# Optimization experiments

Measured on AMD Instinct MI355X. Metric: run time of the kernel, lower is better.

Reference implementation:

```python
import jax, jax.numpy as jnp
import numpy as np

C = 128; HEADS = 8; GH = 32; GW = 32; B = 8; PD = 8  # PD = (dim//4)//4

def _conv(x, w, pad, dil=1, groups=1):
    return jax.lax.conv_general_dilated(
        x, w, (1, 1), [(pad[0], pad[0]), (pad[1], pad[1])],
        rhs_dilation=(dil, dil),
        dimension_numbers=('NCHW', 'OIHW', 'NCHW'),
        feature_group_count=groups)

def _lrelu(t):
    return jnp.where(t >= 0, t, 0.1 * t)

def _ln(t, g, b, eps=1e-5):
    m = jnp.mean(t, -1, keepdims=True)
    v = jnp.var(t, -1, keepdims=True)
    return (t - m) * jax.lax.rsqrt(v + eps) * g + b

def setup_inputs():
    rng = np.random.RandomState(0)
    f = lambda *s: jnp.asarray((rng.randn(*s) * 0.05).astype(np.float32))
    ones = lambda n: jnp.ones((n,), jnp.float32)
    zeros = lambda n: jnp.zeros((n,), jnp.float32)
    # Swin-style relative position index over the (GH, GW) group
    coords = np.stack(np.meshgrid(np.arange(GH), np.arange(GW), indexing='ij')).reshape(2, -1)
    rel = (coords[:, :, None] - coords[:, None, :]).transpose(1, 2, 0)
    rel[..., 0] += GH - 1; rel[..., 1] += GW - 1; rel[..., 0] *= 2 * GW - 1
    rel_idx = jnp.asarray(rel.sum(-1).astype(np.int32))  # [N, N]
    biases = np.stack(np.meshgrid(np.arange(1 - GH, GH), np.arange(1 - GW, GW), indexing='ij'))
    biases = jnp.asarray(biases.reshape(2, -1).T.astype(np.float32))  # [(2GH-1)*(2GW-1), 2]
    return dict(
        x=jnp.asarray(rng.rand(B, C, GH, GW).astype(np.float32)),
        conv1_w=f(C, C, 3, 3), conv2_w=f(C, C, 3, 3), conv3_w=f(C, C, 3, 3),
        convt_w=f(C, 3, 1, 1),
        rba_w=f(C, C, 3, 1), rba_b=zeros(C), rbb_w=f(C, C, 1, 3), rbb_b=zeros(C),
        pp_w=f(PD, 2), pp_b=zeros(PD),
        l1_g=ones(PD), l1_b=zeros(PD), l1_w=f(PD, PD), l1_b2=zeros(PD),
        l2_g=ones(PD), l2_b=zeros(PD), l2_w=f(PD, PD), l2_b2=zeros(PD),
        l3_g=ones(PD), l3_b=zeros(PD), l3_w=f(HEADS, PD), l3_b2=zeros(HEADS),
        qk_w=f(2 * C, C), qk_b=zeros(2 * C),
        v_w=f(C, C), v_b=zeros(C),
        proj_w=f(C, C), proj_b=zeros(C),
        fc1_w=f(C, C), fc1_b=zeros(C), fc2_w=f(C, C), fc2_b=zeros(C),
        biases=biases, rel_idx=rel_idx,
    )

def reference(x, conv1_w, conv2_w, conv3_w, convt_w, rba_w, rba_b, rbb_w, rbb_b,
              pp_w, pp_b, l1_g, l1_b, l1_w, l1_b2, l2_g, l2_b, l2_w, l2_b2,
              l3_g, l3_b, l3_w, l3_b2, qk_w, qk_b, v_w, v_b, proj_w, proj_b,
              fc1_w, fc1_b, fc2_w, fc2_b, biases, rel_idx):
    Bn, Cc, Hh, Ww = x.shape
    N = Hh * Ww
    hd = Cc // HEADS
    # FeaExtract: ResASPP (3 dilated 3x3 convs, grouped 1x1 merge) + residual
    b1 = _lrelu(_conv(x, conv1_w, (1, 1)))
    b2 = _lrelu(_conv(x, conv2_w, (3, 3), dil=3))
    b3 = _lrelu(_conv(x, conv3_w, (5, 5), dil=5))
    a = _conv(jnp.concatenate([b1, b2, b3], 1), convt_w, (0, 0), groups=Cc) + x
    # RB: (3,1) conv -> lrelu -> (1,3) conv + residual
    r = _lrelu(_conv(a, rba_w, (1, 0)) + rba_b[None, :, None, None])
    r = _conv(r, rbb_w, (0, 1)) + rbb_b[None, :, None, None]
    o0 = r + a
    # original uses in-place clamp_, so o0 is clamped before flattening
    o0 = jnp.clip(o0, 0.0, 1.0)
    E = o0.reshape(Bn, Cc, N).transpose(0, 2, 1)  # [B, N, C]
    qk = E @ qk_w.T + qk_b  # [B, N, 2C]
    q = qk[..., :Cc].reshape(Bn, N, HEADS, hd).transpose(0, 2, 1, 3)
    k = qk[..., Cc:].reshape(Bn, N, HEADS, hd).transpose(0, 2, 1, 3)
    v = (E @ v_w.T + v_b).reshape(Bn, N, HEADS, hd).transpose(0, 2, 1, 3)
    attn = jnp.einsum('bhid,bhjd->bhij', q * (hd ** -0.5), k)
    # DynamicPosBias MLP (residual=False): Linear(2,pd) -> [LN,ReLU,Linear] x2 -> LN,ReLU,Linear(pd,heads)
    p = biases @ pp_w.T + pp_b
    p = jax.nn.relu(_ln(p, l1_g, l1_b)) @ l1_w.T + l1_b2
    p = jax.nn.relu(_ln(p, l2_g, l2_b)) @ l2_w.T + l2_b2
    p = jax.nn.relu(_ln(p, l3_g, l3_b)) @ l3_w.T + l3_b2  # [L, heads]
    rpb = p[rel_idx]  # gather -> [N, N, heads]
    attn = attn + rpb.transpose(2, 0, 1)[None]
    attn = jax.nn.softmax(attn, axis=-1)
    y = jnp.einsum('bhij,bhjd->bhid', attn, v).transpose(0, 2, 1, 3).reshape(Bn, N, Cc) + E
    x_proj = y @ proj_w.T + proj_b
    h = jax.nn.gelu(x_proj @ fc1_w.T + fc1_b, approximate=False)
    return (h @ fc2_w.T + fc2_b) + y
```

## Files before the change

### kernel.cpp

```cpp
#include <hip/hip_runtime.h>
#include <hip/hip_bf16.h>

typedef __hip_bfloat16 bf16;
typedef __bf16 bf16x8 __attribute__((ext_vector_type(8)));
typedef float f32x4 __attribute__((ext_vector_type(4)));

#define Lb 3969

#define XP_F   0
#define WF_F   903168
#define WR_F   1124352
#define WG_F   1173504
#define BH_F   1222656
#define R1P_F  1222656
#define QKV_F  1222656
#define AP_F   2795520
#define YT_F   2795520
#define EB_F   3352576
#define XPT_F  3352576
#define H1T_F  0
#define RPB_F  3876864
#define FLAG_F 3908616
#define RT_F   3908624
#define VT_F   4924432

__device__ __forceinline__ float b2f(bf16 v) { return __bfloat162float(v); }
__device__ __forceinline__ bf16 f2b(float v) { return __float2bfloat16(v); }

template <typename T> __device__ __forceinline__ float ldw(const void* p, int i);
template <> __device__ __forceinline__ float ldw<bf16>(const void* p, int i) {
  return __bfloat162float(((const bf16*)p)[i]);
}
template <> __device__ __forceinline__ float ldw<float>(const void* p, int i) {
  return ((const float*)p)[i];
}
template <typename T> __device__ __forceinline__ void stw(void* p, size_t i, float v);
template <> __device__ __forceinline__ void stw<bf16>(void* p, size_t i, float v) {
  ((bf16*)p)[i] = __float2bfloat16(v);
}
template <> __device__ __forceinline__ void stw<float>(void* p, size_t i, float v) {
  ((float*)p)[i] = v;
}

__device__ __forceinline__ unsigned pkb(float a, float b) {
  bf16 x = __float2bfloat16(a), y = __float2bfloat16(b);
  unsigned short ux = *(unsigned short*)&x, uy = *(unsigned short*)&y;
  return (unsigned)ux | ((unsigned)uy << 16);
}

__device__ __forceinline__ bool detect_local(const unsigned* x) {
  int lane = threadIdx.x & 63;
  int cnt = 0;
#pragma unroll
  for (int k = 0; k < 4; ++k) {
// ... 39 lines not shown
            f2b(ldw<T>(w, ((mt * 16 + li) * 128 + Kc * 32 + quad * 8 + j) * 3 + t));
    } else if (u < 24576) {
      int g = u - 12288;
      int Kc = (g >> 6) & 3, mtg = g >> 8;
      const void* w; int mrow; float sc = 1.f;
      if (mtg < 16)      { w = qk_w;   mrow = mtg * 16; if (mtg < 8) sc = 0.25f; }
      else if (mtg < 24) { w = v_w;    mrow = (mtg - 16) * 16; }
      else if (mtg < 32) { w = proj_w; mrow = (mtg - 24) * 16; }
      else if (mtg < 40) { w = fc1_w;  mrow = (mtg - 32) * 16; }
      else               { w = fc2_w;  mrow = (mtg - 40) * 16; }
#pragma unroll
      for (int j = 0; j < 8; ++j)
        Wg[(size_t)g * 8 + j] =
            f2b(sc * ldw<T>(w, (mrow + li) * 128 + Kc * 32 + quad * 8 + j));
    }
  }
}

__global__ __launch_bounds__(256) void wprep_all_kernel(
    const unsigned* x, const void* w1, const void* w2, const void* w3,
    const void* rba_w, const void* rbb_w, const void* qk_w, const void* v_w,
    const void* proj_w, const void* fc1_w, const void* fc2_w,
    bf16* Wf, bf16* Wr, bf16* Wg, int* flag)
{
  bool isbf = detect_local(x);
  if (blockIdx.x == 0 && threadIdx.x == 0) *flag = isbf ? 1 : 0;
  if (isbf) wprep_all_body<bf16>(w1, w2, w3, rba_w, rbb_w, qk_w, v_w, proj_w,
                                 fc1_w, fc2_w, Wf, Wr, Wg);
  else      wprep_all_body<float>(w1, w2, w3, rba_w, rbb_w, qk_w, v_w, proj_w,
                                  fc1_w, fc2_w, Wf, Wr, Wg);
}

template <typename T>
__device__ void nhwc_body(const void* x, bf16* __restrict__ xp, bf16 (*tile)[128])
{
  const int b = blockIdx.x >> 5;
  const int row = blockIdx.x & 31;
  const int t = threadIdx.x;
  const size_t bbase = (size_t)b * 42 * 42 * 128;
  const bf16x8 z = (bf16x8){};

  if (t < 160) {
    int side = t / 80;
    int off = (t % 80) * 8;
    *(bf16x8*)&xp[bbase + ((size_t)(row + 5) * 42 + side * 37) * 128 + off] = z;
  }
  {
    int zr = (row < 5) ? row : ((row >= 27) ? row + 10 : -1);
    if (zr >= 0) {
      size_t base = bbase + (size_t)zr * 42 * 128;
      for (int k = t; k < 672; k += 256) *(bf16x8*)&xp[base + k * 8] = z;
    }
  }

  {
    int ci = t >> 1, half = t & 1;
#pragma unroll
    for (int j = 0; j < 16; ++j) {
      int px = half * 16 + j;
      tile[px][ci] = f2b(ldw<T>(x, ((size_t)b * 128 + ci) * 1024 + row * 32 + px));
    }
  }
  __syncthreads();
  {
    int px = t >> 3, c0 = (t & 7) * 16;
    bf16* dst = xp + (bbase + ((size_t)(row + 5) * 42 + (px + 5)) * 128 + c0);
// ... 73 lines not shown
  const int y = px >> 5, x = px & 31;
  const bf16* brow = bh + ((size_t)b * 1024 + px) * 384 + o0 * 3;
  const bf16* xrow = xp + (((size_t)b * 42 + y + 5) * 42 + x + 5) * 128 + o0;
  bf16* arow = ap + (((size_t)b * 34 + y + 1) * 32 + x) * 128 + o0;

  bf16 bl[48], xl[16], ol[16];
#pragma unroll
  for (int k = 0; k < 6; ++k) *(bf16x8*)&bl[k * 8] = *(const bf16x8*)&brow[k * 8];
  *(bf16x8*)&xl[0] = *(const bf16x8*)&xrow[0];
  *(bf16x8*)&xl[8] = *(const bf16x8*)&xrow[8];
#pragma unroll
  for (int j = 0; j < 16; ++j) {
    float v = b2f(xl[j]);
#pragma unroll
    for (int i = 0; i < 3; ++i) {
      float t = b2f(bl[j * 3 + i]);
      v += cw[(o0 + j) * 3 + i] * (t >= 0.f ? t : 0.1f * t);
    }
    ol[j] = f2b(v);
  }
  *(bf16x8*)&arow[0] = *(bf16x8*)&ol[0];
  *(bf16x8*)&arow[8] = *(bf16x8*)&ol[8];
}

__global__ __launch_bounds__(256) void merge2_kernel(
    const bf16* xp, const void* wt, const bf16* bh, bf16* ap, const int* flag)
{
  __shared__ float cw[384];
  if (*flag) merge2_body<bf16>(xp, wt, bh, ap, cw);
  else       merge2_body<float>(xp, wt, bh, ap, cw);
}

template <typename T>
__device__ void rb1_body(const bf16* __restrict__ ap, const bf16* __restrict__ Wr,
                         const void* bias, bf16* __restrict__ r1p)
{
  const int b = blockIdx.z, mh = blockIdx.y;
  const int lane = threadIdx.x;
  const int quad = lane >> 4, li = lane & 15;
  const int pxw = blockIdx.x * 16;
  const int y = pxw >> 5, xb = pxw & 31;
  f32x4 acc[4] = {};
#pragma unroll
  for (int t = 0; t < 3; ++t) {
    const bf16* Asite = ap + (((size_t)b * 34 + y + t) * 32 + xb + li) * 128;
#pragma unroll
    for (int Kc = 0; Kc < 4; ++Kc) {
      bf16x8 afrag = *(const bf16x8*)(Asite + Kc * 32 + quad * 8);
#pragma unroll
      for (int mt = 0; mt < 4; ++mt) {
        int f = (t * 8 + mh * 4 + mt) * 4 + Kc;
        bf16x8 wfrag = *(const bf16x8*)(Wr + ((size_t)f * 64 + lane) * 8);
        acc[mt] = __builtin_amdgcn_mfma_f32_16x16x32_bf16(afrag, wfrag, acc[mt],
                                                          0, 0, 0);
      }
    }
  }
  if (quad == 0) {
    int xcol = (xb == 0) ? 0 : 33;
#pragma unroll
    for (int mt = 0; mt < 4; ++mt)
      r1p[(((size_t)b * 32 + y) * 34 + xcol) * 128 + (mh * 4 + mt) * 16 + li] =
          f2b(0.f);
  }
#pragma unroll
  for (int mt = 0; mt < 4; ++mt) {
    int o = (mh * 4 + mt) * 16 + li;
    float bv = ldw<T>(bias, o);
#pragma unroll
    for (int r = 0; r < 4; ++r) {
      int x = xb + quad * 4 + r;
      float v = acc[mt][r] + bv;
      v = (v >= 0.f ? v : 0.1f * v);
      r1p[(((size_t)b * 32 + y) * 34 + x + 1) * 128 + o] = f2b(v);
    }
  }
}

__global__ __launch_bounds__(64) void rb1_kernel(
    const bf16* ap, const bf16* Wr, const void* bias, bf16* r1p, const int* flag)
{
  if (*flag) rb1_body<bf16>(ap, Wr, bias, r1p);
  else       rb1_body<float>(ap, Wr, bias, r1p);
}

template <typename T>
__device__ void rb2_body(const bf16* __restrict__ r1p, const bf16* __restrict__ Wr,
                         const void* bias, const bf16* __restrict__ ap,
                         bf16* __restrict__ Eb)
{
  const int b = blockIdx.z, mh = blockIdx.y;
  const int lane = threadIdx.x;
  const int quad = lane >> 4, li = lane & 15;
  const int pxw = blockIdx.x * 16;
  const int y = pxw >> 5, xb = pxw & 31;
  f32x4 acc[4] = {};
#pragma unroll
  for (int t = 0; t < 3; ++t) {
    const bf16* Asite = r1p + (((size_t)b * 32 + y) * 34 + xb + li + t) * 128;
#pragma unroll
    for (int Kc = 0; Kc < 4; ++Kc) {
      bf16x8 afrag = *(const bf16x8*)(Asite + Kc * 32 + quad * 8);
#pragma unroll
      for (int mt = 0; mt < 4; ++mt) {
        int f = ((3 + t) * 8 + mh * 4 + mt) * 4 + Kc;
        bf16x8 wfrag = *(const bf16x8*)(Wr + ((size_t)f * 64 + lane) * 8);
        acc[mt] = __builtin_amdgcn_mfma_f32_16x16x32_bf16(afrag, wfrag, acc[mt],
                                                          0, 0, 0);
      }
    }
  }
#pragma unroll
  for (int mt = 0; mt < 4; ++mt) {
    int o = (mh * 4 + mt) * 16 + li;
    float bv = ldw<T>(bias, o);
#pragma unroll
    for (int r = 0; r < 4; ++r) {
      int x = xb + quad * 4 + r;
      float v = acc[mt][r] + bv +
                b2f(ap[(((size_t)b * 34 + y + 1) * 32 + x) * 128 + o]);
      v = fminf(fmaxf(v, 0.f), 1.f);
      Eb[((size_t)b * 1024 + y * 32 + x) * 128 + o] = f2b(v);
    }
  }
}

__global__ __launch_bounds__(64) void rb2_kernel(
    const bf16* r1p, const bf16* Wr, const void* bias, const bf16* ap,
    bf16* Eb, const int* flag)
{
  if (*flag) rb2_body<bf16>(r1p, Wr, bias, ap, Eb);
  else       rb2_body<float>(r1p, Wr, bias, ap, Eb);
}

template <typename T>
__device__ __forceinline__ void ln_relu8(const float* t, float* u,
                                         const void* g, const void* bb)
{
  float m = 0.f;
#pragma unroll
  for (int k = 0; k < 8; ++k) m += t[k];
  m *= 0.125f;
  float v = 0.f;
#pragma unroll
  for (int k = 0; k < 8; ++k) { float d = t[k] - m; v += d * d; }
  v *= 0.125f;
  float r = rsqrtf(v + 1e-5f);
#pragma unroll
  for (int k = 0; k < 8; ++k) {
    float val = (t[k] - m) * r * ldw<T>(g, k) + ldw<T>(bb, k);
    u[k] = val > 0.f ? val : 0.f;
  }
}

template <typename T>
__device__ void dpb_body(const void* biases, const void* pp_w, const void* pp_b,
                         const void* l1_g, const void* l1_b, const void* l1_w,
                         const void* l1_b2, const void* l2_g, const void* l2_b,
                         const void* l2_w, const void* l2_b2, const void* l3_g,
                         const void* l3_b, const void* l3_w, const void* l3_b2,
                         float* __restrict__ RPB)
{
  int r = blockIdx.x * 256 + threadIdx.x;
  if (r >= Lb) return;
  float b0 = ldw<T>(biases, r * 2), b1 = ldw<T>(biases, r * 2 + 1);
  float t[8], u[8];
#pragma unroll
  for (int j = 0; j < 8; ++j)
    t[j] = b0 * ldw<T>(pp_w, j * 2) + b1 * ldw<T>(pp_w, j * 2 + 1) +
           ldw<T>(pp_b, j);
  ln_relu8<T>(t, u, l1_g, l1_b);
#pragma unroll
  for (int j = 0; j < 8; ++j) {
    float s = ldw<T>(l1_b2, j);
#pragma unroll
    for (int k = 0; k < 8; ++k) s += u[k] * ldw<T>(l1_w, j * 8 + k);
    t[j] = s;
  }
  ln_relu8<T>(t, u, l2_g, l2_b);
#pragma unroll
  for (int j = 0; j < 8; ++j) {
    float s = ldw<T>(l2_b2, j);
#pragma unroll
    for (int k = 0; k < 8; ++k) s += u[k] * ldw<T>(l2_w, j * 8 + k);
    t[j] = s;
  }
  ln_relu8<T>(t, u, l3_g, l3_b);
#pragma unroll
  for (int h = 0; h < 8; ++h) {
    float s = ldw<T>(l3_b2, h);
#pragma unroll
    for (int k = 0; k < 8; ++k) s += u[k] * ldw<T>(l3_w, h * 8 + k);
    RPB[h * Lb + r] = s;
  }
}

__global__ __launch_bounds__(256) void dpb_kernel(
    const void* biases, const void* pp_w, const void* pp_b, const void* l1_g,
    const void* l1_b, const void* l1_w, const void* l1_b2, const void* l2_g,
    const void* l2_b, const void* l2_w, const void* l2_b2, const void* l3_g,
    const void* l3_b, const void* l3_w, const void* l3_b2, float* RPB,
    const int* flag)
{
  if (*flag)
    dpb_body<bf16>(biases, pp_w, pp_b, l1_g, l1_b, l1_w, l1_b2, l2_g, l2_b,
                   l2_w, l2_b2, l3_g, l3_b, l3_w, l3_b2, RPB);
  else
    dpb_body<float>(biases, pp_w, pp_b, l1_g, l1_b, l1_w, l1_b2, l2_g, l2_b,
                    l2_w, l2_b2, l3_g, l3_b, l3_w, l3_b2, RPB);
}

__global__ __launch_bounds__(64) void rt_kernel(
    const float* __restrict__ RPB, float* __restrict__ RT)
{
  const int tt = blockIdx.x, h = blockIdx.y;
  const int t = tt >> 1, p = tt & 1;
  const int lane = threadIdx.x, quad = lane >> 4, li = lane & 15;
  const float* rp = RPB + h * Lb;
#pragma unroll
  for (int mt = 0; mt < 4; ++mt) {
    f32x4 v;
#pragma unroll
    for (int r = 0; r < 4; ++r) {
      int j = mt * 16 + quad * 4 + r;
      int dy = (t - 30) - (j >> 5);
      int dx = (p * 16 + li) - (j & 31);
      v[r] = rp[(dy + 31) * 63 + dx + 31];
    }
    *(f32x4*)&RT[(((size_t)h * 124 + tt) * 4 + mt) * 256 + lane * 4] = v;
  }
}

__global__ __launch_bounds__(64) void vt_kernel(
    const bf16* __restrict__ QKV, bf16* __restrict__ VT)
{
  const int c = blockIdx.x, hh = blockIdx.y, b = blockIdx.z;
  __shared__ bf16 Vl[64][20];
  const int lane = threadIdx.x, quad = lane >> 4, li = lane & 15;
  const bf16* vsrc =
      QKV + ((size_t)b * 1024 + c * 64 + lane) * 384 + 256 + hh * 16;
  union { bf16x8 v; uint2 u[2]; } w0, w1;
  w0.v = *(const bf16x8*)vsrc;
  w1.v = *(const bf16x8*)(vsrc + 8);
  *(uint2*)&Vl[lane][0] = w0.u[0];
  *(uint2*)&Vl[lane][4] = w0.u[1];
  *(uint2*)&Vl[lane][8] = w1.u[0];
  *(uint2*)&Vl[lane][12] = w1.u[1];
  __syncthreads();
#pragma unroll
  for (int half = 0; half < 2; ++half) {
    union { bf16 e[8]; bf16x8 v; } uv;
#pragma unroll
    for (int jj = 0; jj < 8; ++jj)
      uv.e[jj] = Vl[half * 32 + quad * 8 + jj][li];
    *(bf16x8*)&VT[((((size_t)(b * 8 + hh) * 16 + c) * 2 + half) * 64 + lane) * 8] =
        uv.v;
  }
}

template <typename T>
__device__ void qkv_body(const bf16* __restrict__ Eb, const bf16* __restrict__ Wg,
                         const void* qk_b, const void* v_b,
                         bf16* __restrict__ QKV)
{
  const int grp = blockIdx.y, b = blockIdx.z;
  const int w = threadIdx.x >> 6, lane = threadIdx.x & 63;
  const int quad = lane >> 4, li = lane & 15;
  const int pxw = blockIdx.x * 64 + w * 16;
  bf16x8 ef[4];
#pragma unroll
  for (int Kc = 0; Kc < 4; ++Kc)
    ef[Kc] = *(const bf16x8*)&Eb[((size_t)b * 1024 + pxw + li) * 128 + Kc * 32 +
                                 quad * 8];
  f32x4 acc[8] = {};
#pragma unroll
  for (int nt = 0; nt < 8; ++nt) {
    int g = grp * 8 + nt;
#pragma unroll
    for (int Kc = 0; Kc < 4; ++Kc) {
      bf16x8 wf = *(const bf16x8*)&Wg[(((size_t)g * 4 + Kc) * 64 + lane) * 8];
      acc[nt] = __builtin_amdgcn_mfma_f32_16x16x32_bf16(ef[Kc], wf, acc[nt],
                                                        0, 0, 0);
    }
  }
#pragma unroll
  for (int nt = 0; nt < 8; ++nt) {
    int g = grp * 8 + nt;
    int o = g * 16 + li;
    float bv;
    if (g < 8)       bv = 0.25f * ldw<T>(qk_b, o);
    else if (g < 16) bv = ldw<T>(qk_b, o);
    else             bv = ldw<T>(v_b, o - 256);
#pragma unroll
    for (int r = 0; r < 4; ++r) {
      int px = pxw + quad * 4 + r;
      QKV[((size_t)b * 1024 + px) * 384 + o] = f2b(acc[nt][r] + bv);
    }
  }
}

__global__ __launch_bounds__(256) void qkv_kernel(
    const bf16* Eb, const bf16* Wg, const void* qk_b, const void* v_b,
    bf16* QKV, const int* flag)
{
  if (*flag) qkv_body<bf16>(Eb, Wg, qk_b, v_b, QKV);
  else       qkv_body<float>(Eb, Wg, qk_b, v_b, QKV);
}

template <typename T, int MODE>
__device__ void mlp_body(const bf16* __restrict__ src, const bf16* __restrict__ Wg,
                         int tb, const void* bias, const bf16* __restrict__ res,
                         void* out)
{
  const int b = blockIdx.z, mh = blockIdx.y;
  const int lane = threadIdx.x;
  const int quad = lane >> 4, li = lane & 15;
  const int pxw = blockIdx.x * 16;
  bf16x8 ef[4];
#pragma unroll
  for (int Kc = 0; Kc < 4; ++Kc)
    ef[Kc] = *(const bf16x8*)&src[((size_t)b * 1024 + pxw + li) * 128 + Kc * 32 +
                                  quad * 8];
  f32x4 acc[2] = {};
#pragma unroll
  for (int nt = 0; nt < 2; ++nt)
#pragma unroll
    for (int Kc = 0; Kc < 4; ++Kc) {
      bf16x8 wf = *(const bf16x8*)&Wg[
          (((size_t)(tb + mh * 2 + nt) * 4 + Kc) * 64 + lane) * 8];
      acc[nt] = __builtin_amdgcn_mfma_f32_16x16x32_bf16(ef[Kc], wf, acc[nt],
                                                        0, 0, 0);
    }
#pragma unroll
  for (int nt = 0; nt < 2; ++nt) {
    int o = (mh * 2 + nt) * 16 + li;
    float bv = ldw<T>(bias, o);
#pragma unroll
    for (int r = 0; r < 4; ++r) {
      int px = pxw + quad * 4 + r;
      float v = acc[nt][r] + bv;
      size_t oidx = ((size_t)b * 1024 + px) * 128 + o;
      if (MODE == 1) v = 0.5f * v * (1.f + erff(v * 0.70710678118f));
      if (MODE == 2) {
        v += b2f(res[oidx]);
        stw<T>(out, oidx, v);
      } else {
        ((bf16*)out)[oidx] = f2b(v);
      }
    }
  }
}

template <int MODE>
__global__ __launch_bounds__(64) void mlp_kernel(
    const bf16* src, const bf16* Wg, int tb, const void* bias, const bf16* res,
    void* out, const int* flag)
{
  if (*flag) mlp_body<bf16, MODE>(src, Wg, tb, bias, res, out);
  else       mlp_body<float, MODE>(src, Wg, tb, bias, res, out);
}

__global__ __launch_bounds__(64) void attn_kernel(
    const bf16* __restrict__ QKV, const bf16* __restrict__ Eb,
    const float* __restrict__ RT, const bf16* __restrict__ VT,
    bf16* __restrict__ Yt)
{
  const int qt = blockIdx.x;
  const int hh = blockIdx.y;
  const int b = blockIdx.z;

  __shared__ bf16 Pl[16][72];

  const int lane = threadIdx.x;
  const int quad = lane >> 4, li = lane & 15;
  const int qb = qt * 16;

  const bf16* QKVb = QKV + (size_t)b * 1024 * 384;
  const bf16* VTb = VT + (size_t)(b * 8 + hh) * 16 * 1024;
  const float* RTh = RT + (size_t)hh * 124 * 1024;

  bf16x8 qf = (bf16x8){};
  if (quad < 2)
    qf = *(const bf16x8*)&QKVb[(size_t)(qb + li) * 384 + hh * 16 + quad * 8];

  f32x4 O_ = {};
  float lsum = 0.f;
  const int sbase = (lane & 48) + ((lane >> 2) & 12);

  for (int c = 0; c < 16; ++c) {
    const int c0 = c * 64;
    const int tt = ((qt >> 1) - 2 * c + 30) * 2 + (qt & 1);
    const float* rtp = RTh + (size_t)tt * 1024 + lane * 4;

    f32x4 sT[4];
#pragma unroll
    for (int mt = 0; mt < 4; ++mt) {
      f32x4 cin = *(const f32x4*)(rtp + (size_t)mt * 256);
      bf16x8 kf = (bf16x8){};
      if (quad < 2)
        kf = *(const bf16x8*)&QKVb[(size_t)(c0 + mt * 16 + li) * 384 + 128 +
                                   hh * 16 + quad * 8];
      sT[mt] = __builtin_amdgcn_mfma_f32_16x16x32_bf16(kf, qf, cin, 0, 0, 0);
    }

#pragma unroll
    for (int mt = 0; mt < 4; ++mt)
#pragma unroll
      for (int r = 0; r < 4; ++r) {
        float p = __expf(sT[mt][r]);
        sT[mt][r] = p;
        lsum += p;
      }

#pragma unroll
    for (int mt = 0; mt < 4; ++mt) {
      uint2 w;
      w.x = pkb(sT[mt][0], sT[mt][1]);
      w.y = pkb(sT[mt][2], sT[mt][3]);
      *(uint2*)&Pl[li][mt * 16 + quad * 4] = w;
    }

#pragma unroll
    for (int half = 0; half < 2; ++half) {
      bf16x8 vf = *(const bf16x8*)&VTb[((size_t)(c * 2 + half) * 64 + lane) * 8];
      bf16x8 pf = *(const bf16x8*)&Pl[li][half * 32 + quad * 8];
      O_ = __builtin_amdgcn_mfma_f32_16x16x32_bf16(pf, vf, O_, 0, 0, 0);
    }
  }

  lsum += __shfl_xor(lsum, 16);
  lsum += __shfl_xor(lsum, 32);

  const bf16* Ebp = Eb + (size_t)b * 1024 * 128 + hh * 16 + li;
  bf16* Ytp = Yt + (size_t)b * 1024 * 128 + hh * 16 + li;
#pragma unroll
  for (int r = 0; r < 4; ++r) {
    float lb = __shfl(lsum, sbase + r);
    int qrow = qb + quad * 4 + r;
    Ytp[(size_t)qrow * 128] =
        f2b(O_[r] / lb + b2f(Ebp[(size_t)qrow * 128]));
  }
}

extern "C" void kernel_launch(void* const* d_in, const int* in_sizes, int n_in,
                              void* d_out, int out_size, void* d_ws,
                              size_t ws_size, hipStream_t stream)
{
  (void)in_sizes; (void)n_in; (void)out_size; (void)ws_size;
  const void* x       = d_in[0];
  const void* conv1_w = d_in[1];
  const void* conv2_w = d_in[2];
  const void* conv3_w = d_in[3];
  const void* convt_w = d_in[4];
  const void* rba_w   = d_in[5];
  const void* rba_b   = d_in[6];
  const void* rbb_w   = d_in[7];
  const void* rbb_b   = d_in[8];
  const void* pp_w    = d_in[9];
  const void* pp_b    = d_in[10];
  const void* l1_g    = d_in[11];
  const void* l1_b    = d_in[12];
  const void* l1_w    = d_in[13];
  const void* l1_b2   = d_in[14];
  const void* l2_g    = d_in[15];
  const void* l2_b    = d_in[16];
  const void* l2_w    = d_in[17];
  const void* l2_b2   = d_in[18];
  const void* l3_g    = d_in[19];
  const void* l3_b    = d_in[20];
  const void* l3_w    = d_in[21];
  const void* l3_b2   = d_in[22];
  const void* qk_w    = d_in[23];
  const void* qk_b    = d_in[24];
  const void* v_w     = d_in[25];
  const void* v_b     = d_in[26];
  const void* proj_w  = d_in[27];
  const void* proj_b  = d_in[28];
  const void* fc1_w   = d_in[29];
  const void* fc1_b   = d_in[30];
  const void* fc2_w   = d_in[31];
  const void* fc2_b   = d_in[32];
  const void* biases  = d_in[33];

  float* ws   = (float*)d_ws;
  bf16*  xp   = (bf16*)(ws + XP_F);
  bf16*  Wf   = (bf16*)(ws + WF_F);
  bf16*  Wr   = (bf16*)(ws + WR_F);
  bf16*  Wg   = (bf16*)(ws + WG_F);
  bf16*  bh   = (bf16*)(ws + BH_F);
  bf16*  r1p  = (bf16*)(ws + R1P_F);
  bf16*  QKV  = (bf16*)(ws + QKV_F);
  bf16*  ap   = (bf16*)(ws + AP_F);
  bf16*  Yt   = (bf16*)(ws + YT_F);
  bf16*  Eb   = (bf16*)(ws + EB_F);
  bf16*  XPt  = (bf16*)(ws + XPT_F);
  bf16*  H1t  = (bf16*)(ws + H1T_F);
  float* RPB  = ws + RPB_F;
  int*   flag = (int*)(ws + FLAG_F);
  float* RT   = ws + RT_F;
  bf16*  VT   = (bf16*)(ws + VT_F);

  wprep_all_kernel<<<312, 256, 0, stream>>>(
      (const unsigned*)x, conv1_w, conv2_w, conv3_w, rba_w, rbb_w, qk_w, v_w,
      proj_w, fc1_w, fc2_w, Wf, Wr, Wg, flag);
  nhwc_kernel<<<256, 256, 0, stream>>>(x, xp, flag);
  aspp2_kernel<<<dim3(16, 6, 8), 256, 0, stream>>>(xp, Wf, bh);
  merge2_kernel<<<dim3(32, 8), 256, 0, stream>>>(xp, convt_w, bh, ap, flag);
  rb1_kernel<<<dim3(64, 2, 8), 64, 0, stream>>>(ap, Wr, rba_b, r1p, flag);
  rb2_kernel<<<dim3(64, 2, 8), 64, 0, stream>>>(r1p, Wr, rbb_b, ap, Eb, flag);
  dpb_kernel<<<16, 256, 0, stream>>>(biases, pp_w, pp_b, l1_g, l1_b, l1_w,
                                     l1_b2, l2_g, l2_b, l2_w, l2_b2, l3_g,
                                     l3_b, l3_w, l3_b2, RPB, flag);
  rt_kernel<<<dim3(124, 8), 64, 0, stream>>>(RPB, RT);
  qkv_kernel<<<dim3(16, 3, 8), 256, 0, stream>>>(Eb, Wg, qk_b, v_b, QKV, flag);
  vt_kernel<<<dim3(16, 8, 8), 64, 0, stream>>>(QKV, VT);
  attn_kernel<<<dim3(64, 8, 8), 64, 0, stream>>>(QKV, Eb, RT, VT, Yt);
  mlp_kernel<0><<<dim3(64, 4, 8), 64, 0, stream>>>(Yt, Wg, 24, proj_b, nullptr,
                                                   XPt, flag);
  mlp_kernel<1><<<dim3(64, 4, 8), 64, 0, stream>>>(XPt, Wg, 32, fc1_b, nullptr,
                                                   H1t, flag);
  mlp_kernel<2><<<dim3(64, 4, 8), 64, 0, stream>>>(H1t, Wg, 40, fc2_b, Yt,
                                                   d_out, flag);
}
```

Before: 245.6 us.

## Fuse residual convs, DPB+RT, and MLP chain; split attention keys across two waves

Merges rb1/rb2 into one kernel that keeps the intermediate row in LDS, so r1p no longer goes through global memory. dpb and rt are merged into a single kernel that evaluates the MLP only for the table entries each tile needs, and this runs early in the launch sequence. The three MLP GEMMs are merged into one kernel with LDS staging. Attention now uses two waves per block, each covering half the key chunks, and combines their partial results through LDS. Together these cut launches and global round trips, but the fused kernels run fewer blocks and hold more accumulators per thread, which can lower occupancy.

```diff
diff --git a/kernel.cpp b/kernel.cpp
--- a/kernel.cpp
+++ b/kernel.cpp
@@ -12,14 +12,10 @@
 #define WR_F   1124352
 #define WG_F   1173504
 #define BH_F   1222656
-#define R1P_F  1222656
 #define QKV_F  1222656
 #define AP_F   2795520
 #define YT_F   2795520
 #define EB_F   3352576
-#define XPT_F  3352576
-#define H1T_F  0
-#define RPB_F  3876864
 #define FLAG_F 3908616
 #define RT_F   3908624
 #define VT_F   4924432
@@ -125,6 +121,106 @@
 }
 
 template <typename T>
+__device__ __forceinline__ void ln_relu8(const float* t, float* u,
+                                         const void* g, const void* bb)
+{
+  float m = 0.f;
+#pragma unroll
+  for (int k = 0; k < 8; ++k) m += t[k];
+  m *= 0.125f;
+  float v = 0.f;
+#pragma unroll
+  for (int k = 0; k < 8; ++k) { float d = t[k] - m; v += d * d; }
+  v *= 0.125f;
+  float r = rsqrtf(v + 1e-5f);
+#pragma unroll
+  for (int k = 0; k < 8; ++k) {
+    float val = (t[k] - m) * r * ldw<T>(g, k) + ldw<T>(bb, k);
+    u[k] = val > 0.f ? val : 0.f;
+  }
+}
+
+template <typename T>
+__device__ void dpbrt_body(const void* biases, const void* pp_w, const void* pp_b,
+    const void* l1_g, const void* l1_b, const void* l1_w, const void* l1_b2,
+    const void* l2_g, const void* l2_b, const void* l2_w, const void* l2_b2,
+    const void* l3_g, const void* l3_b, const void* l3_w, const void* l3_b2,
+    float* __restrict__ RT, float (*LH)[47][8])
+{
+  const int tt = blockIdx.x, t = tt >> 1, p = tt & 1;
+  const int lane = threadIdx.x, quad = lane >> 4, li = lane & 15;
+
+  for (int it = 0; it < 2; ++it) {
+    int idx = it * 64 + lane;
+    if (idx < 94) {
+      int sd = idx / 47, xi = idx - sd * 47;
+      int rtab = (t + 1 - sd) * 63 + p * 16 + xi;
+      float b0 = ldw<T>(biases, rtab * 2), b1 = ldw<T>(biases, rtab * 2 + 1);
+      float tv[8], u[8];
+#pragma unroll
+      for (int j = 0; j < 8; ++j)
+        tv[j] = b0 * ldw<T>(pp_w, j * 2) + b1 * ldw<T>(pp_w, j * 2 + 1) +
+                ldw<T>(pp_b, j);
+      ln_relu8<T>(tv, u, l1_g, l1_b);
+#pragma unroll
+      for (int j = 0; j < 8; ++j) {
+        float s = ldw<T>(l1_b2, j);
+#pragma unroll
+        for (int k = 0; k < 8; ++k) s += u[k] * ldw<T>(l1_w, j * 8 + k);
+        tv[j] = s;
+      }
+      ln_relu8<T>(tv, u, l2_g, l2_b);
+#pragma unroll
+      for (int j = 0; j < 8; ++j) {
+        float s = ldw<T>(l2_b2, j);
+#pragma unroll
+        for (int k = 0; k < 8; ++k) s += u[k] * ldw<T>(l2_w, j * 8 + k);
+        tv[j] = s;
+      }
+      ln_relu8<T>(tv, u, l3_g, l3_b);
+#pragma unroll
+      for (int h = 0; h < 8; ++h) {
+        float s = ldw<T>(l3_b2, h);
+#pragma unroll
+        for (int k = 0; k < 8; ++k) s += u[k] * ldw<T>(l3_w, h * 8 + k);
+        LH[sd][xi][h] = s;
+      }
+    }
+  }
+  __syncthreads();
+#pragma unroll
+  for (int h = 0; h < 8; ++h)
+#pragma unroll
+    for (int mt = 0; mt < 4; ++mt) {
+      f32x4 v;
+#pragma unroll
+      for (int r = 0; r < 4; ++r) {
+        int j = mt * 16 + quad * 4 + r;
+        int jy = j >> 5;
+        int xi = li + 31 - (j & 31);
+        v[r] = LH[jy][xi][h];
+      }
+      *(f32x4*)&RT[(((size_t)h * 124 + tt) * 4 + mt) * 256 + lane * 4] = v;
+    }
+}
+
+__global__ __launch_bounds__(64) void dpbrt_kernel(
+    const void* biases, const void* pp_w, const void* pp_b, const void* l1_g,
+    const void* l1_b, const void* l1_w, const void* l1_b2, const void* l2_g,
+    const void* l2_b, const void* l2_w, const void* l2_b2, const void* l3_g,
+    const void* l3_b, const void* l3_w, const void* l3_b2, float* RT,
+    const int* flag)
+{
+  __shared__ float LH[2][47][8];
+  if (*flag)
+    dpbrt_body<bf16>(biases, pp_w, pp_b, l1_g, l1_b, l1_w, l1_b2, l2_g, l2_b,
+                     l2_w, l2_b2, l3_g, l3_b, l3_w, l3_b2, RT, LH);
+  else
+    dpbrt_body<float>(biases, pp_w, pp_b, l1_g, l1_b, l1_w, l1_b2, l2_g, l2_b,
+                      l2_w, l2_b2, l3_g, l3_b, l3_w, l3_b2, RT, LH);
+}
+
+template <typename T>
 __device__ void nhwc_body(const void* x, bf16* __restrict__ xp, bf16 (*tile)[128])
 {
   const int b = blockIdx.x >> 5;
@@ -264,15 +360,16 @@
 }
 
 template <typename T>
-__device__ void rb1_body(const bf16* __restrict__ ap, const bf16* __restrict__ Wr,
-                         const void* bias, bf16* __restrict__ r1p)
-{
-  const int b = blockIdx.z, mh = blockIdx.y;
-  const int lane = threadIdx.x;
+__device__ void rbf_body(const bf16* __restrict__ ap, const bf16* __restrict__ Wr,
+                         const void* rba_b, const void* rbb_b,
+                         bf16* __restrict__ Eb, bf16 (*Lr)[136])
+{
+  const int y = blockIdx.x, b = blockIdx.y;
+  const int w = threadIdx.x >> 6, lane = threadIdx.x & 63;
   const int quad = lane >> 4, li = lane & 15;
-  const int pxw = blockIdx.x * 16;
-  const int y = pxw >> 5, xb = pxw & 31;
-  f32x4 acc[4] = {};
+  const int xb = w * 16;
+
+  f32x4 acc[8] = {};
 #pragma unroll
   for (int t = 0; t < 3; ++t) {
     const bf16* Asite = ap + (((size_t)b * 34 + y + t) * 32 + xb + li) * 128;
@@ -280,76 +377,51 @@
     for (int Kc = 0; Kc < 4; ++Kc) {
       bf16x8 afrag = *(const bf16x8*)(Asite + Kc * 32 + quad * 8);
 #pragma unroll
-      for (int mt = 0; mt < 4; ++mt) {
-        int f = (t * 8 + mh * 4 + mt) * 4 + Kc;
+      for (int mt = 0; mt < 8; ++mt) {
+        int f = (t * 8 + mt) * 4 + Kc;
         bf16x8 wfrag = *(const bf16x8*)(Wr + ((size_t)f * 64 + lane) * 8);
         acc[mt] = __builtin_amdgcn_mfma_f32_16x16x32_bf16(afrag, wfrag, acc[mt],
                                                           0, 0, 0);
       }
     }
   }
-  if (quad == 0) {
-    int xcol = (xb == 0) ? 0 : 33;
-#pragma unroll
-    for (int mt = 0; mt < 4; ++mt)
-      r1p[(((size_t)b * 32 + y) * 34 + xcol) * 128 + (mh * 4 + mt) * 16 + li] =
-          f2b(0.f);
-  }
-#pragma unroll
-  for (int mt = 0; mt < 4; ++mt) {
-    int o = (mh * 4 + mt) * 16 + li;
-    float bv = ldw<T>(bias, o);
+  *(unsigned*)&Lr[w * 33][lane * 2] = 0u;
+#pragma unroll
+  for (int mt = 0; mt < 8; ++mt) {
+    int o = mt * 16 + li;
+    float bv = ldw<T>(rba_b, o);
+#pragma unroll
+    for (int r = 0; r < 4; ++r) {
+      float v = acc[mt][r] + bv;
+      v = (v >= 0.f ? v : 0.1f * v);
+      Lr[xb + quad * 4 + r + 1][o] = f2b(v);
+    }
+  }
+  __syncthreads();
+
+  f32x4 acc2[8] = {};
+#pragma unroll
+  for (int t = 0; t < 3; ++t) {
+#pragma unroll
+    for (int Kc = 0; Kc < 4; ++Kc) {
+      bf16x8 afrag = *(const bf16x8*)&Lr[xb + li + t][Kc * 32 + quad * 8];
+#pragma unroll
+      for (int mt = 0; mt < 8; ++mt) {
+        int f = ((3 + t) * 8 + mt) * 4 + Kc;
+        bf16x8 wfrag = *(const bf16x8*)(Wr + ((size_t)f * 64 + lane) * 8);
+        acc2[mt] = __builtin_amdgcn_mfma_f32_16x16x32_bf16(afrag, wfrag, acc2[mt],
+                                                           0, 0, 0);
+      }
+    }
+  }
+#pragma unroll
+  for (int mt = 0; mt < 8; ++mt) {
+    int o = mt * 16 + li;
+    float bv = ldw<T>(rbb_b, o);
 #pragma unroll
     for (int r = 0; r < 4; ++r) {
       int x = xb + quad * 4 + r;
-      float v = acc[mt][r] + bv;
-      v = (v >= 0.f ? v : 0.1f * v);
-      r1p[(((size_t)b * 32 + y) * 34 + x + 1) * 128 + o] = f2b(v);
-    }
-  }
-}
-
-__global__ __launch_bounds__(64) void rb1_kernel(
-    const bf16* ap, const bf16* Wr, const void* bias, bf16* r1p, const int* flag)
-{
-  if (*flag) rb1_body<bf16>(ap, Wr, bias, r1p);
-  else       rb1_body<float>(ap, Wr, bias, r1p);
-}
-
-template <typename T>
-__device__ void rb2_body(const bf16* __restrict__ r1p, const bf16* __restrict__ Wr,
-                         const void* bias, const bf16* __restrict__ ap,
-                         bf16* __restrict__ Eb)
-{
-  const int b = blockIdx.z, mh = blockIdx.y;
-  const int lane = threadIdx.x;
-  const int quad = lane >> 4, li = lane & 15;
-  const int pxw = blockIdx.x * 16;
-  const int y = pxw >> 5, xb = pxw & 31;
-  f32x4 acc[4] = {};
-#pragma unroll
-  for (int t = 0; t < 3; ++t) {
-    const bf16* Asite = r1p + (((size_t)b * 32 + y) * 34 + xb + li + t) * 128;
-#pragma unroll
-    for (int Kc = 0; Kc < 4; ++Kc) {
-      bf16x8 afrag = *(const bf16x8*)(Asite + Kc * 32 + quad * 8);
-#pragma unroll
-      for (int mt = 0; mt < 4; ++mt) {
-        int f = ((3 + t) * 8 + mh * 4 + mt) * 4 + Kc;
-        bf16x8 wfrag = *(const bf16x8*)(Wr + ((size_t)f * 64 + lane) * 8);
-        acc[mt] = __builtin_amdgcn_mfma_f32_16x16x32_bf16(afrag, wfrag, acc[mt],
-                                                          0, 0, 0);
-      }
-    }
-  }
-#pragma unroll
-  for (int mt = 0; mt < 4; ++mt) {
-    int o = (mh * 4 + mt) * 16 + li;
-    float bv = ldw<T>(bias, o);
-#pragma unroll
-    for (int r = 0; r < 4; ++r) {
-      int x = xb + quad * 4 + r;
-      float v = acc[mt][r] + bv +
+      float v = acc2[mt][r] + bv +
                 b2f(ap[(((size_t)b * 34 + y + 1) * 32 + x) * 128 + o]);
       v = fminf(fmaxf(v, 0.f), 1.f);
       Eb[((size_t)b * 1024 + y * 32 + x) * 128 + o] = f2b(v);
@@ -357,110 +429,62 @@
   }
 }
 
-__global__ __launch_bounds__(64) void rb2_kernel(
-    const bf16* r1p, const bf16* Wr, const void* bias, const bf16* ap,
+__global__ __launch_bounds__(128) void rbf_kernel(
+    const bf16* ap, const bf16* Wr, const void* rba_b, const void* rbb_b,
     bf16* Eb, const int* flag)
 {
-  if (*flag) rb2_body<bf16>(r1p, Wr, bias, ap, Eb);
-  else       rb2_body<float>(r1p, Wr, bias, ap, Eb);
+  __shared__ bf16 Lr[34][136];
+  if (*flag) rbf_body<bf16>(ap, Wr, rba_b, rbb_b, Eb, Lr);
+  else       rbf_body<float>(ap, Wr, rba_b, rbb_b, Eb, Lr);
 }
 
 template <typename T>
-__device__ __forceinline__ void ln_relu8(const float* t, float* u,
-                                         const void* g, const void* bb)
-{
-  float m = 0.f;
-#pragma unroll
-  for (int k = 0; k < 8; ++k) m += t[k];
-  m *= 0.125f;
-  float v = 0.f;
-#pragma unroll
-  for (int k = 0; k < 8; ++k) { float d = t[k] - m; v += d * d; }
-  v *= 0.125f;
-  float r = rsqrtf(v + 1e-5f);
-#pragma unroll
-  for (int k = 0; k < 8; ++k) {
-    float val = (t[k] - m) * r * ldw<T>(g, k) + ldw<T>(bb, k);
-    u[k] = val > 0.f ? val : 0.f;
-  }
-}
-
-template <typename T>
-__device__ void dpb_body(const void* biases, const void* pp_w, const void* pp_b,
-                         const void* l1_g, const void* l1_b, const void* l1_w,
-                         const void* l1_b2, const void* l2_g, const void* l2_b,
-                         const void* l2_w, const void* l2_b2, const void* l3_g,
-                         const void* l3_b, const void* l3_w, const void* l3_b2,
-                         float* __restrict__ RPB)
-{
-  int r = blockIdx.x * 256 + threadIdx.x;
-  if (r >= Lb) return;
-  float b0 = ldw<T>(biases, r * 2), b1 = ldw<T>(biases, r * 2 + 1);
-  float t[8], u[8];
-#pragma unroll
-  for (int j = 0; j < 8; ++j)
-    t[j] = b0 * ldw<T>(pp_w, j * 2) + b1 * ldw<T>(pp_w, j * 2 + 1) +
-           ldw<T>(pp_b, j);
-  ln_relu8<T>(t, u, l1_g, l1_b);
-#pragma unroll
-  for (int j = 0; j < 8; ++j) {
-    float s = ldw<T>(l1_b2, j);
-#pragma unroll
-    for (int k = 0; k < 8; ++k) s += u[k] * ldw<T>(l1_w, j * 8 + k);
-    t[j] = s;
-  }
-  ln_relu8<T>(t, u, l2_g, l2_b);
-#pragma unroll
-  for (int j = 0; j < 8; ++j) {
-    float s = ldw<T>(l2_b2, j);
-#pragma unroll
-    for (int k = 0; k < 8; ++k) s += u[k] * ldw<T>(l2_w, j * 8 + k);
-    t[j] = s;
-  }
-  ln_relu8<T>(t, u, l3_g, l3_b);
-#pragma unroll
-  for (int h = 0; h < 8; ++h) {
-    float s = ldw<T>(l3_b2, h);
-#pragma unroll
-    for (int k = 0; k < 8; ++k) s += u[k] * ldw<T>(l3_w, h * 8 + k);
-    RPB[h * Lb + r] = s;
-  }
-}
-
-__global__ __launch_bounds__(256) void dpb_kernel(
-    const void* biases, const void* pp_w, const void* pp_b, const void* l1_g,
-    const void* l1_b, const void* l1_w, const void* l1_b2, const void* l2_g,
-    const void* l2_b, const void* l2_w, const void* l2_b2, const void* l3_g,
-    const void* l3_b, const void* l3_w, const void* l3_b2, float* RPB,
-    const int* flag)
-{
-  if (*flag)
-    dpb_body<bf16>(biases, pp_w, pp_b, l1_g, l1_b, l1_w, l1_b2, l2_g, l2_b,
-                   l2_w, l2_b2, l3_g, l3_b, l3_w, l3_b2, RPB);
-  else
-    dpb_body<float>(biases, pp_w, pp_b, l1_g, l1_b, l1_w, l1_b2, l2_g, l2_b,
-                    l2_w, l2_b2, l3_g, l3_b, l3_w, l3_b2, RPB);
-}
-
-__global__ __launch_bounds__(64) void rt_kernel(
-    const float* __restrict__ RPB, float* __restrict__ RT)
-{
-  const int tt = blockIdx.x, h = blockIdx.y;
-  const int t = tt >> 1, p = tt & 1;
-  const int lane = threadIdx.x, quad = lane >> 4, li = lane & 15;
-  const float* rp = RPB + h * Lb;
-#pragma unroll
-  for (int mt = 0; mt < 4; ++mt) {
-    f32x4 v;
+__device__ void qkv_body(const bf16* __restrict__ Eb, const bf16* __restrict__ Wg,
+                         const void* qk_b, const void* v_b,
+                         bf16* __restrict__ QKV)
+{
+  const int grp = blockIdx.y, b = blockIdx.z;
+  const int w = threadIdx.x >> 6, lane = threadIdx.x & 63;
+  const int quad = lane >> 4, li = lane & 15;
+  const int pxw = blockIdx.x * 64 + w * 16;
+  bf16x8 ef[4];
+#pragma unroll
+  for (int Kc = 0; Kc < 4; ++Kc)
+    ef[Kc] = *(const bf16x8*)&Eb[((size_t)b * 1024 + pxw + li) * 128 + Kc * 32 +
+                                 quad * 8];
+  f32x4 acc[8] = {};
+#pragma unroll
+  for (int nt = 0; nt < 8; ++nt) {
+    int g = grp * 8 + nt;
+#pragma unroll
+    for (int Kc = 0; Kc < 4; ++Kc) {
+      bf16x8 wf = *(const bf16x8*)&Wg[(((size_t)g * 4 + Kc) * 64 + lane) * 8];
+      acc[nt] = __builtin_amdgcn_mfma_f32_16x16x32_bf16(ef[Kc], wf, acc[nt],
+                                                        0, 0, 0);
+    }
+  }
+#pragma unroll
+  for (int nt = 0; nt < 8; ++nt) {
+    int g = grp * 8 + nt;
+    int o = g * 16 + li;
+    float bv;
+    if (g < 8)       bv = 0.25f * ldw<T>(qk_b, o);
+    else if (g < 16) bv = ldw<T>(qk_b, o);
+    else             bv = ldw<T>(v_b, o - 256);
 #pragma unroll
     for (int r = 0; r < 4; ++r) {
-      int j = mt * 16 + quad * 4 + r;
-      int dy = (t - 30) - (j >> 5);
-      int dx = (p * 16 + li) - (j & 31);
-      v[r] = rp[(dy + 31) * 63 + dx + 31];
-    }
-    *(f32x4*)&RT[(((size_t)h * 124 + tt) * 4 + mt) * 256 + lane * 4] = v;
-  }
+      int px = pxw + quad * 4 + r;
+      QKV[((size_t)b * 1024 + px) * 384 + o] = f2b(acc[nt][r] + bv);
+    }
+  }
+}
+
+__global__ __launch_bounds__(256) void qkv_kernel(
+    const bf16* Eb, const bf16* Wg, const void* qk_b, const void* v_b,
+    bf16* QKV, const int* flag)
+{
+  if (*flag) qkv_body<bf16>(Eb, Wg, qk_b, v_b, QKV);
+  else       qkv_body<float>(Eb, Wg, qk_b, v_b, QKV);
 }
 
 __global__ __launch_bounds__(64) void vt_kernel(
@@ -490,109 +514,7 @@
   }
 }
 
-template <typename T>
-__device__ void qkv_body(const bf16* __restrict__ Eb, const bf16* __restrict__ Wg,
-                         const void* qk_b, const void* v_b,
-                         bf16* __restrict__ QKV)
-{
-  const int grp = blockIdx.y, b = blockIdx.z;
-  const int w = threadIdx.x >> 6, lane = threadIdx.x & 63;
-  const int quad = lane >> 4, li = lane & 15;
-  const int pxw = blockIdx.x * 64 + w * 16;
-  bf16x8 ef[4];
-#pragma unroll
-  for (int Kc = 0; Kc < 4; ++Kc)
-    ef[Kc] = *(const bf16x8*)&Eb[((size_t)b * 1024 + pxw + li) * 128 + Kc * 32 +
-                                 quad * 8];
-  f32x4 acc[8] = {};
-#pragma unroll
-  for (int nt = 0; nt < 8; ++nt) {
-    int g = grp * 8 + nt;
-#pragma unroll
-    for (int Kc = 0; Kc < 4; ++Kc) {
-      bf16x8 wf = *(const bf16x8*)&Wg[(((size_t)g * 4 + Kc) * 64 + lane) * 8];
-      acc[nt] = __builtin_amdgcn_mfma_f32_16x16x32_bf16(ef[Kc], wf, acc[nt],
-                                                        0, 0, 0);
-    }
-  }
-#pragma unroll
-  for (int nt = 0; nt < 8; ++nt) {
-    int g = grp * 8 + nt;
-    int o = g * 16 + li;
-    float bv;
-    if (g < 8)       bv = 0.25f * ldw<T>(qk_b, o);
-    else if (g < 16) bv = ldw<T>(qk_b, o);
-    else             bv = ldw<T>(v_b, o - 256);
-#pragma unroll
-    for (int r = 0; r < 4; ++r) {
-      int px = pxw + quad * 4 + r;
-      QKV[((size_t)b * 1024 + px) * 384 + o] = f2b(acc[nt][r] + bv);
-    }
-  }
-}
-
-__global__ __launch_bounds__(256) void qkv_kernel(
-    const bf16* Eb, const bf16* Wg, const void* qk_b, const void* v_b,
-    bf16* QKV, const int* flag)
-{
-  if (*flag) qkv_body<bf16>(Eb, Wg, qk_b, v_b, QKV);
-  else       qkv_body<float>(Eb, Wg, qk_b, v_b, QKV);
-}
-
-template <typename T, int MODE>
-__device__ void mlp_body(const bf16* __restrict__ src, const bf16* __restrict__ Wg,
-                         int tb, const void* bias, const bf16* __restrict__ res,
-                         void* out)
-{
-  const int b = blockIdx.z, mh = blockIdx.y;
-  const int lane = threadIdx.x;
-  const int quad = lane >> 4, li = lane & 15;
-  const int pxw = blockIdx.x * 16;
-  bf16x8 ef[4];
-#pragma unroll
-  for (int Kc = 0; Kc < 4; ++Kc)
-    ef[Kc] = *(const bf16x8*)&src[((size_t)b * 1024 + pxw + li) * 128 + Kc * 32 +
-                                  quad * 8];
-  f32x4 acc[2] = {};
-#pragma unroll
-  for (int nt = 0; nt < 2; ++nt)
-#pragma unroll
-    for (int Kc = 0; Kc < 4; ++Kc) {
-      bf16x8 wf = *(const bf16x8*)&Wg[
-          (((size_t)(tb + mh * 2 + nt) * 4 + Kc) * 64 + lane) * 8];
-      acc[nt] = __builtin_amdgcn_mfma_f32_16x16x32_bf16(ef[Kc], wf, acc[nt],
-                                                        0, 0, 0);
-    }
-#pragma unroll
-  for (int nt = 0; nt < 2; ++nt) {
-    int o = (mh * 2 + nt) * 16 + li;
-    float bv = ldw<T>(bias, o);
-#pragma unroll
-    for (int r = 0; r < 4; ++r) {
-      int px = pxw + quad * 4 + r;
-      float v = acc[nt][r] + bv;
-      size_t oidx = ((size_t)b * 1024 + px) * 128 + o;
-      if (MODE == 1) v = 0.5f * v * (1.f + erff(v * 0.70710678118f));
-      if (MODE == 2) {
-        v += b2f(res[oidx]);
-        stw<T>(out, oidx, v);
-      } else {
-        ((bf16*)out)[oidx] = f2b(v);
-      }
-    }
-  }
-}
-
-template <int MODE>
-__global__ __launch_bounds__(64) void mlp_kernel(
-    const bf16* src, const bf16* Wg, int tb, const void* bias, const bf16* res,
-    void* out, const int* flag)
-{
-  if (*flag) mlp_body<bf16, MODE>(src, Wg, tb, bias, res, out);
-  else       mlp_body<float, MODE>(src, Wg, tb, bias, res, out);
-}
-
-__global__ __launch_bounds__(64) void attn_kernel(
+__global__ __launch_bounds__(128) void attn_kernel(
     const bf16* __restrict__ QKV, const bf16* __restrict__ Eb,
     const float* __restrict__ RT, const bf16* __restrict__ VT,
     bf16* __restrict__ Yt)
@@ -601,9 +523,10 @@
   const int hh = blockIdx.y;
   const int b = blockIdx.z;
 
-  __shared__ bf16 Pl[16][72];
-
-  const int lane = threadIdx.x;
+  __shared__ bf16 Pl[2][16][72];
+  __shared__ float Red[64][5];
+
+  const int w = threadIdx.x >> 6, lane = threadIdx.x & 63;
   const int quad = lane >> 4, li = lane & 15;
   const int qb = qt * 16;
 
@@ -617,9 +540,9 @@
 
   f32x4 O_ = {};
   float lsum = 0.f;
-  const int sbase = (lane & 48) + ((lane >> 2) & 12);
-
-  for (int c = 0; c < 16; ++c) {
+
+  for (int cc = 0; cc < 8; ++cc) {
+    const int c = w * 8 + cc;
     const int c0 = c * 64;
     const int tt = ((qt >> 1) - 2 * c + 30) * 2 + (qt & 1);
     const float* rtp = RTh + (size_t)tt * 1024 + lane * 4;
@@ -646,32 +569,135 @@
 
 #pragma unroll
     for (int mt = 0; mt < 4; ++mt) {
-      uint2 w;
-      w.x = pkb(sT[mt][0], sT[mt][1]);
-      w.y = pkb(sT[mt][2], sT[mt][3]);
-      *(uint2*)&Pl[li][mt * 16 + quad * 4] = w;
+      uint2 ww;
+      ww.x = pkb(sT[mt][0], sT[mt][1]);
+      ww.y = pkb(sT[mt][2], sT[mt][3]);
+      *(uint2*)&Pl[w][li][mt * 16 + quad * 4] = ww;
     }
 
 #pragma unroll
     for (int half = 0; half < 2; ++half) {
       bf16x8 vf = *(const bf16x8*)&VTb[((size_t)(c * 2 + half) * 64 + lane) * 8];
-      bf16x8 pf = *(const bf16x8*)&Pl[li][half * 32 + quad * 8];
+      bf16x8 pf = *(const bf16x8*)&Pl[w][li][half * 32 + quad * 8];
       O_ = __builtin_amdgcn_mfma_f32_16x16x32_bf16(pf, vf, O_, 0, 0, 0);
     }
   }
 
-  lsum += __shfl_xor(lsum, 16);
-  lsum += __shfl_xor(lsum, 32);
-
-  const bf16* Ebp = Eb + (size_t)b * 1024 * 128 + hh * 16 + li;
-  bf16* Ytp = Yt + (size_t)b * 1024 * 128 + hh * 16 + li;
-#pragma unroll
-  for (int r = 0; r < 4; ++r) {
-    float lb = __shfl(lsum, sbase + r);
-    int qrow = qb + quad * 4 + r;
-    Ytp[(size_t)qrow * 128] =
-        f2b(O_[r] / lb + b2f(Ebp[(size_t)qrow * 128]));
-  }
+  if (w == 1) {
+#pragma unroll
+    for (int r = 0; r < 4; ++r) Red[lane][r] = O_[r];
+    Red[lane][4] = lsum;
+  }
+  __syncthreads();
+  if (w == 0) {
+#pragma unroll
+    for (int r = 0; r < 4; ++r) O_[r] += Red[lane][r];
+    lsum += Red[lane][4];
+    lsum += __shfl_xor(lsum, 16);
+    lsum += __shfl_xor(lsum, 32);
+    const int sbase = (lane & 48) + ((lane >> 2) & 12);
+    const bf16* Ebp = Eb + (size_t)b * 1024 * 128 + hh * 16 + li;
+    bf16* Ytp = Yt + (size_t)b * 1024 * 128 + hh * 16 + li;
+#pragma unroll
+    for (int r = 0; r < 4; ++r) {
+      float lb = __shfl(lsum, sbase + r);
+      int qrow = qb + quad * 4 + r;
+      Ytp[(size_t)qrow * 128] =
+          f2b(O_[r] / lb + b2f(Ebp[(size_t)qrow * 128]));
+    }
+  }
+}
+
+template <typename T>
+__device__ void mlpf_body(const bf16* __restrict__ Yt, const bf16* __restrict__ Wg,
+                          const void* proj_b, const void* fc1_b,
+                          const void* fc2_b, void* out, bf16 (*Tl)[136])
+{
+  const int b = blockIdx.y;
+  const int lane = threadIdx.x, quad = lane >> 4, li = lane & 15;
+  const int pxw = blockIdx.x * 16;
+
+  bf16x8 ef[4];
+#pragma unroll
+  for (int Kc = 0; Kc < 4; ++Kc)
+    ef[Kc] = *(const bf16x8*)&Yt[((size_t)b * 1024 + pxw + li) * 128 + Kc * 32 +
+                                 quad * 8];
+  f32x4 acc[8] = {};
+#pragma unroll
+  for (int nt = 0; nt < 8; ++nt)
+#pragma unroll
+    for (int Kc = 0; Kc < 4; ++Kc) {
+      bf16x8 wf = *(const bf16x8*)&Wg[(((size_t)(24 + nt) * 4 + Kc) * 64 + lane) * 8];
+      acc[nt] = __builtin_amdgcn_mfma_f32_16x16x32_bf16(ef[Kc], wf, acc[nt],
+                                                        0, 0, 0);
+    }
+#pragma unroll
+  for (int nt = 0; nt < 8; ++nt) {
+    float bv = ldw<T>(proj_b, nt * 16 + li);
+#pragma unroll
+    for (int r = 0; r < 4; ++r)
+      Tl[quad * 4 + r][nt * 16 + li] = f2b(acc[nt][r] + bv);
+  }
+  bf16x8 af[4];
+#pragma unroll
+  for (int Kc = 0; Kc < 4; ++Kc)
+    af[Kc] = *(const bf16x8*)&Tl[li][Kc * 32 + quad * 8];
+
+#pragma unroll
+  for (int nt = 0; nt < 8; ++nt) acc[nt] = (f32x4){};
+#pragma unroll
+  for (int nt = 0; nt < 8; ++nt)
+#pragma unroll
+    for (int Kc = 0; Kc < 4; ++Kc) {
+      bf16x8 wf = *(const bf16x8*)&Wg[(((size_t)(32 + nt) * 4 + Kc) * 64 + lane) * 8];
+      acc[nt] = __builtin_amdgcn_mfma_f32_16x16x32_bf16(af[Kc], wf, acc[nt],
+                                                        0, 0, 0);
+    }
+#pragma unroll
+  for (int nt = 0; nt < 8; ++nt) {
+    float bv = ldw<T>(fc1_b, nt * 16 + li);
+#pragma unroll
+    for (int r = 0; r < 4; ++r) {
+      float v = acc[nt][r] + bv;
+      v = 0.5f * v * (1.f + erff(v * 0.70710678118f));
+      Tl[quad * 4 + r][nt * 16 + li] = f2b(v);
+    }
+  }
+#pragma unroll
+  for (int Kc = 0; Kc < 4; ++Kc)
+    af[Kc] = *(const bf16x8*)&Tl[li][Kc * 32 + quad * 8];
+
+#pragma unroll
+  for (int nt = 0; nt < 8; ++nt) acc[nt] = (f32x4){};
+#pragma unroll
+  for (int nt = 0; nt < 8; ++nt)
+#pragma unroll
+    for (int Kc = 0; Kc < 4; ++Kc) {
+      bf16x8 wf = *(const bf16x8*)&Wg[(((size_t)(40 + nt) * 4 + Kc) * 64 + lane) * 8];
+      acc[nt] = __builtin_amdgcn_mfma_f32_16x16x32_bf16(af[Kc], wf, acc[nt],
+                                                        0, 0, 0);
+    }
+#pragma unroll
+  for (int nt = 0; nt < 8; ++nt) {
+    int o = nt * 16 + li;
+    float bv = ldw<T>(fc2_b, o);
+#pragma unroll
+    for (int r = 0; r < 4; ++r) {
+      int px = pxw + quad * 4 + r;
+      size_t oidx = ((size_t)b * 1024 + px) * 128 + o;
+      float v = acc[nt][r] + bv + b2f(Yt[oidx]);
+      stw<T>(out, oidx, v);
+    }
+  }
+}
+
+__global__ __launch_bounds__(64) void mlpf_kernel(
+    const bf16* Yt, const bf16* Wg, const void* proj_b, const void* fc1_b,
+    const void* fc2_b, void* out, const int* flag)
+{
+  __shared__ bf16 Tl[16][136];
+  if (*flag) mlpf_body<bf16>(Yt, Wg, proj_b, fc1_b, fc2_b, out, Tl);
+  else       mlpf_body<float>(Yt, Wg, proj_b, fc1_b, fc2_b, out, Tl);
 }
 
 extern "C" void kernel_launch(void* const* d_in, const int* in_sizes, int n_in,
@@ -720,14 +746,10 @@
   bf16*  Wr   = (bf16*)(ws + WR_F);
   bf16*  Wg   = (bf16*)(ws + WG_F);
   bf16*  bh   = (bf16*)(ws + BH_F);
-  bf16*  r1p  = (bf16*)(ws + R1P_F);
   bf16*  QKV  = (bf16*)(ws + QKV_F);
   bf16*  ap   = (bf16*)(ws + AP_F);
   bf16*  Yt   = (bf16*)(ws + YT_F);
   bf16*  Eb   = (bf16*)(ws + EB_F);
-  bf16*  XPt  = (bf16*)(ws + XPT_F);
-  bf16*  H1t  = (bf16*)(ws + H1T_F);
-  float* RPB  = ws + RPB_F;
   int*   flag = (int*)(ws + FLAG_F);
   float* RT   = ws + RT_F;
   bf16*  VT   = (bf16*)(ws + VT_F);
@@ -735,22 +757,16 @@
   wprep_all_kernel<<<312, 256, 0, stream>>>(
       (const unsigned*)x, conv1_w, conv2_w, conv3_w, rba_w, rbb_w, qk_w, v_w,
       proj_w, fc1_w, fc2_w, Wf, Wr, Wg, flag);
+  dpbrt_kernel<<<124, 64, 0, stream>>>(biases, pp_w, pp_b, l1_g, l1_b, l1_w,
+                                       l1_b2, l2_g, l2_b, l2_w, l2_b2, l3_g,
+                                       l3_b, l3_w, l3_b2, RT, flag);
   nhwc_kernel<<<256, 256, 0, stream>>>(x, xp, flag);
   aspp2_kernel<<<dim3(16, 6, 8), 256, 0, stream>>>(xp, Wf, bh);
   merge2_kernel<<<dim3(32, 8), 256, 0, stream>>>(xp, convt_w, bh, ap, flag);
-  rb1_kernel<<<dim3(64, 2, 8), 64, 0, stream>>>(ap, Wr, rba_b, r1p, flag);
-  rb2_kernel<<<dim3(64, 2, 8), 64, 0, stream>>>(r1p, Wr, rbb_b, ap, Eb, flag);
-  dpb_kernel<<<16, 256, 0, stream>>>(biases, pp_w, pp_b, l1_g, l1_b, l1_w,
-                                     l1_b2, l2_g, l2_b, l2_w, l2_b2, l3_g,
-                                     l3_b, l3_w, l3_b2, RPB, flag);
-  rt_kernel<<<dim3(124, 8), 64, 0, stream>>>(RPB, RT);
+  rbf_kernel<<<dim3(32, 8), 128, 0, stream>>>(ap, Wr, rba_b, rbb_b, Eb, flag);
   qkv_kernel<<<dim3(16, 3, 8), 256, 0, stream>>>(Eb, Wg, qk_b, v_b, QKV, flag);
   vt_kernel<<<dim3(16, 8, 8), 64, 0, stream>>>(QKV, VT);
-  attn_kernel<<<dim3(64, 8, 8), 64, 0, stream>>>(QKV, Eb, RT, VT, Yt);
-  mlp_kernel<0><<<dim3(64, 4, 8), 64, 0, stream>>>(Yt, Wg, 24, proj_b, nullptr,
-                                                   XPt, flag);
-  mlp_kernel<1><<<dim3(64, 4, 8), 64, 0, stream>>>(XPt, Wg, 32, fc1_b, nullptr,
-                                                   H1t, flag);
-  mlp_kernel<2><<<dim3(64, 4, 8), 64, 0, stream>>>(H1t, Wg, 40, fc2_b, Yt,
-                                                   d_out, flag);
-}
+  attn_kernel<<<dim3(64, 8, 8), 128, 0, stream>>>(QKV, Eb, RT, VT, Yt);
+  mlpf_kernel<<<dim3(64, 8), 64, 0, stream>>>(Yt, Wg, proj_b, fc1_b, fc2_b,
+                                              d_out, flag);
+}
```

After: 286.3 us. +16.6%, slower.
